# Kernel optimization log

Measured on AMD Instinct MI355X. Metric: run time of the kernel, lower is better.

The kernel has to match this reference:

```python
import jax, jax.numpy as jnp
import numpy as np

BN_EPS = 1e-5
TAU = 1.0  # gumbel temperature

def setup_inputs() -> dict:
    key = jax.random.key(0)
    ks = jax.random.split(key, 6)
    B, O, F, H, HID = 32, 4096, 256, 8, 128
    x = jax.random.normal(ks[0], (B, O, F), dtype=jnp.float32)
    gumbel_noise = jax.random.gumbel(ks[1], (B, O, H), dtype=jnp.float32)
    W_in = jax.random.normal(ks[2], (F, HID), dtype=jnp.float32) * (1.0 / np.sqrt(F))
    b_in = jnp.zeros((HID,), jnp.float32)
    W_blk = jax.random.normal(ks[3], (HID, HID), dtype=jnp.float32) * (1.0 / np.sqrt(HID))
    b_blk = jnp.zeros((HID,), jnp.float32)
    bn_gamma = jnp.ones((HID,), jnp.float32)
    bn_beta = jnp.zeros((HID,), jnp.float32)
    W_fc = jax.random.normal(ks[4], (HID, H), dtype=jnp.float32) * (1.0 / np.sqrt(HID))
    b_fc = jnp.zeros((H,), jnp.float32)
    return {"x": x, "gumbel_noise": gumbel_noise, "W_in": W_in, "b_in": b_in,
            "W_blk": W_blk, "b_blk": b_blk, "bn_gamma": bn_gamma, "bn_beta": bn_beta,
            "W_fc": W_fc, "b_fc": b_fc}

def reference(x, gumbel_noise, W_in, b_in, W_blk, b_blk, bn_gamma, bn_beta, W_fc, b_fc):
    B, O, F = x.shape
    xf = x.reshape(B * O, F)
    # DynamicNetwork head: input linear + relu, one residual block (Linear+BN+ReLU), fc
    h = jax.nn.relu(xf @ W_in + b_in)  # (B*O, HID)
    z = h @ W_blk + b_blk
    mu = z.mean(axis=0)
    var = z.var(axis=0)  # biased var, matches BatchNorm training normalization
    z = (z - mu) * jax.lax.rsqrt(var + BN_EPS) * bn_gamma + bn_beta
    h = jax.nn.relu(z) + h  # residual
    logits = (h @ W_fc + b_fc).reshape(B, O, -1)  # (B, O, H)
    # mask out zero-norm observations
    mask = (jnp.linalg.norm(x, axis=2) != 0)[..., None].astype(x.dtype)  # (B, O, 1)
    logits = logits * mask
    # gumbel softmax over observation dim (soft)
    w = jax.nn.softmax((logits + gumbel_noise) / TAU, axis=1)  # (B, O, H)
    # weighted sum pooling: algebraically the repeat-multiply-sum in the original
    pooled = jnp.einsum('boh,bof->bhf', w, x)  # (B, H, F)
    return pooled.reshape(B, -1)  # (B, H*F)
```

## Files before the change

kernel.cpp:

```cpp
#include <hip/hip_runtime.h>
#include <math.h>

#define MB_ 131072
#define F_  256
#define HID_ 128
#define H_  8
#define O_  4096
#define B_  32

typedef __attribute__((ext_vector_type(8))) short short8;
typedef __attribute__((ext_vector_type(4))) float f32x4;

static __device__ __forceinline__ unsigned short f2bf(float f) {
    unsigned int u = __float_as_uint(f);
    unsigned int r = (u + 0x7fffu + ((u >> 16) & 1u)) >> 16;
    return (unsigned short)r;
}
static __device__ __forceinline__ float bflo(unsigned int u) {
    return __uint_as_float(u << 16);
}
static __device__ __forceinline__ float bfhi(unsigned int u) {
    return __uint_as_float(u & 0xffff0000u);
}
static __device__ __forceinline__ unsigned int fkey(float f) {
    unsigned int u = __float_as_uint(f);
    return (u & 0x80000000u) ? ~u : (u | 0x80000000u);
}

__global__ __launch_bounds__(256) void k_prep(
    const float* __restrict__ W_in, const float* __restrict__ W_blk,
    unsigned short* __restrict__ WinT, unsigned short* __restrict__ WblkT,
    unsigned int* __restrict__ Mmax)
{
    const int idx = blockIdx.x * 256 + threadIdx.x;
    if (idx < 256) Mmax[idx] = 0u;
    if (idx < 32768) {
        const int n = idx >> 8, k = idx & 255;
        WinT[idx] = f2bf(W_in[(size_t)k * HID_ + n]);
    } else {
        const int i2 = idx - 32768;
        const int n = i2 >> 7, k = i2 & 127;
        WblkT[i2] = f2bf(W_blk[(size_t)k * HID_ + n]);
    }
}

__global__ __launch_bounds__(256) void k_fused(
    const float* __restrict__ x, const unsigned short* __restrict__ WinT,
    const float* __restrict__ b_in,
    const unsigned short* __restrict__ WblkT, const float* __restrict__ b_blk,
    unsigned short* __restrict__ h_out, unsigned short* __restrict__ z_out,
    float* __restrict__ mask_out,
    float* __restrict__ sumP, float* __restrict__ sumsqP)
{
    __shared__ unsigned short smem[128 * 136];
    __shared__ float msum_s[128];
    __shared__ float csum_s[128], csumsq_s[128];
    unsigned short* a_s = smem;
    unsigned short* b_s = smem + 5120;

    const int tid = threadIdx.x;
    const int R0 = blockIdx.x * 128;
    const int lp_r = tid >> 3;
    const int lp_c = tid & 7;
    const int wave = tid >> 6;
    const int wrow = wave >> 1, wcol = wave & 1;
    const int lane = tid & 63;
    const int lm = lane & 15, quad = lane >> 4;

    if (tid < 128) { msum_s[tid] = 0.f; csum_s[tid] = 0.f; csumsq_s[tid] = 0.f; }
    float ms[4] = {0.f, 0.f, 0.f, 0.f};

    f32x4 acc[4][4];
#pragma unroll
    for (int i = 0; i < 4; i++)
#pragma unroll
        for (int j = 0; j < 4; j++) acc[i][j] = (f32x4){0.f, 0.f, 0.f, 0.f};

    for (int kt = 0; kt < 8; kt++) {
#pragma unroll
        for (int p = 0; p < 4; p++) {
            const int r = lp_r + 32 * p;
            const float4 v = *(const float4*)(x + (size_t)(R0 + r) * F_ + kt * 32 + lp_c * 4);
            ms[p] += v.x * v.x + v.y * v.y + v.z * v.z + v.w * v.w;
            ushort4 o;
            o.x = f2bf(v.x); o.y = f2bf(v.y); o.z = f2bf(v.z); o.w = f2bf(v.w);
            *(ushort4*)(&a_s[r * 40 + lp_c * 4]) = o;
        }
#pragma unroll
        for (int p = 0; p < 4; p++) {
            const int n = lp_r + 32 * p;
            const ushort4 wv = *(const ushort4*)(WinT + (size_t)n * F_ + kt * 32 + lp_c * 4);
            *(ushort4*)(&b_s[n * 40 + lp_c * 4]) = wv;
        }
        __syncthreads();
        short8 af[4], bfr[4];
#pragma unroll
        for (int mi = 0; mi < 4; mi++)
            af[mi] = *(const short8*)(&a_s[(wrow * 64 + mi * 16 + lm) * 40 + quad * 8]);
#pragma unroll
        for (int ni = 0; ni < 4; ni++)
            bfr[ni] = *(const short8*)(&b_s[(wcol * 64 + ni * 16 + lm) * 40 + quad * 8]);
#pragma unroll
        for (int mi = 0; mi < 4; mi++)
#pragma unroll
            for (int ni = 0; ni < 4; ni++)
                acc[mi][ni] = __builtin_amdgcn_mfma_f32_16x16x32_bf16(af[mi], bfr[ni], acc[mi][ni], 0, 0, 0);
        __syncthreads();
    }

#pragma unroll
    for (int p = 0; p < 4; p++) atomicAdd(&msum_s[lp_r + 32 * p], ms[p]);

    {
        float bcol[4];
#pragma unroll
        for (int ni = 0; ni < 4; ni++) bcol[ni] = b_in[wcol * 64 + ni * 16 + lm];
#pragma unroll
        for (int mi = 0; mi < 4; mi++)
#pragma unroll
            for (int r = 0; r < 4; r++) {
                const int rl = wrow * 64 + mi * 16 + quad * 4 + r;
                const size_t grow = (size_t)(R0 + rl) * HID_;
#pragma unroll
                for (int ni = 0; ni < 4; ni++) {
                    const int col = wcol * 64 + ni * 16 + lm;
                    const float v = fmaxf(acc[mi][ni][r] + bcol[ni], 0.f);
                    const unsigned short us = f2bf(v);
                    h_out[grow + col] = us;
                    smem[rl * 136 + col] = us;
                }
            }
    }
#pragma unroll
    for (int i = 0; i < 4; i++)
#pragma unroll
        for (int j = 0; j < 4; j++) acc[i][j] = (f32x4){0.f, 0.f, 0.f, 0.f};
    __syncthreads();

    if (tid < 128) mask_out[R0 + tid] = (msum_s[tid] != 0.f) ? 1.f : 0.f;

#pragma unroll
    for (int kt = 0; kt < 4; kt++) {
        short8 af[4], bfr[4];
#pragma unroll
        for (int mi = 0; mi < 4; mi++)
            af[mi] = *(const short8*)(&smem[(wrow * 64 + mi * 16 + lm) * 136 + kt * 32 + quad * 8]);
#pragma unroll
        for (int ni = 0; ni < 4; ni++)
            bfr[ni] = *(const short8*)(WblkT + (size_t)(wcol * 64 + ni * 16 + lm) * HID_ + kt * 32 + quad * 8);
#pragma unroll
        for (int mi = 0; mi < 4; mi++)
#pragma unroll
            for (int ni = 0; ni < 4; ni++)
                acc[mi][ni] = __builtin_amdgcn_mfma_f32_16x16x32_bf16(af[mi], bfr[ni], acc[mi][ni], 0, 0, 0);
    }

    float bcol2[4];
#pragma unroll
    for (int ni = 0; ni < 4; ni++) bcol2[ni] = b_blk[wcol * 64 + ni * 16 + lm];
    float s_c[4] = {0.f, 0.f, 0.f, 0.f}, ss_c[4] = {0.f, 0.f, 0.f, 0.f};
#pragma unroll
    for (int mi = 0; mi < 4; mi++)
#pragma unroll
        for (int r = 0; r < 4; r++) {
            const size_t row = (size_t)R0 + wrow * 64 + mi * 16 + quad * 4 + r;
#pragma unroll
            for (int ni = 0; ni < 4; ni++) {
                const float zv = acc[mi][ni][r] + bcol2[ni];
                s_c[ni] += zv;
                ss_c[ni] += zv * zv;
                z_out[row * HID_ + wcol * 64 + ni * 16 + lm] = f2bf(zv);
            }
        }
#pragma unroll
    for (int ni = 0; ni < 4; ni++) {
        atomicAdd(&csum_s[wcol * 64 + ni * 16 + lm], s_c[ni]);
        atomicAdd(&csumsq_s[wcol * 64 + ni * 16 + lm], ss_c[ni]);
    }
    __syncthreads();
    if (tid < 128) {
        sumP[(size_t)blockIdx.x * 128 + tid] = csum_s[tid];
        sumsqP[(size_t)blockIdx.x * 128 + tid] = csumsq_s[tid];
    }
}

__global__ __launch_bounds__(256) void k_bnfin(
    const float* __restrict__ sumP, const float* __restrict__ sumsqP,
    const float* __restrict__ gamma, const float* __restrict__ beta,
    float* __restrict__ scale, float* __restrict__ shift)
{
    const int c = blockIdx.x;
    const int tid = threadIdx.x;
    float s = 0.f, ss = 0.f;
    for (int i = tid; i < 1024; i += 256) {
        s  += sumP[(size_t)i * 128 + c];
        ss += sumsqP[(size_t)i * 128 + c];
    }
#pragma unroll
    for (int off = 32; off; off >>= 1) {
        s  += __shfl_xor(s, off, 64);
        ss += __shfl_xor(ss, off, 64);
    }
    __shared__ float rs[4], rss[4];
    const int wid = tid >> 6, lane = tid & 63;
    if (lane == 0) { rs[wid] = s; rss[wid] = ss; }
    __syncthreads();
    if (tid == 0) {
        const float S  = rs[0] + rs[1] + rs[2] + rs[3];
        const float SS = rss[0] + rss[1] + rss[2] + rss[3];
        const float inv_m = 1.0f / (float)MB_;
        const float mu = S * inv_m;
        const float var = SS * inv_m - mu * mu;
        const float sc = gamma[c] * rsqrtf(var + 1e-5f);
        scale[c] = sc;
        shift[c] = beta[c] - mu * sc;
    }
}

__global__ __launch_bounds__(256) void k_logits(
    const unsigned short* __restrict__ h_in, const unsigned short* __restrict__ z_in,
    const float* __restrict__ scale, const float* __restrict__ shift,
    const float* __restrict__ W_fc, const float* __restrict__ b_fc,
    const float* __restrict__ mask, const float* __restrict__ gumbel,
    float* __restrict__ t_out, unsigned int* __restrict__ Mmax)
{
    __shared__ float wfc_s[1024];
    __shared__ float sc_s[128], sh_s[128];
    const int tid = threadIdx.x;
    for (int i = tid; i < 1024; i += 256) wfc_s[i] = W_fc[i];
    if (tid < 128) { sc_s[tid] = scale[tid]; sh_s[tid] = shift[tid]; }
    __syncthreads();

    const size_t row0 = (size_t)blockIdx.x * 512 + tid;
    const size_t row1 = row0 + 256;
    float a0[8], a1[8];
#pragma unroll
    for (int j = 0; j < 8; j++) { a0[j] = 0.f; a1[j] = 0.f; }

    const uint4* hp0 = (const uint4*)(h_in + row0 * HID_);
    const uint4* zq0 = (const uint4*)(z_in + row0 * HID_);
    const uint4* hp1 = (const uint4*)(h_in + row1 * HID_);
    const uint4* zq1 = (const uint4*)(z_in + row1 * HID_);

#pragma unroll 2
    for (int kc = 0; kc < 16; kc++) {
        const uint4 h0 = hp0[kc], z0 = zq0[kc];
        const uint4 h1 = hp1[kc], z1 = zq1[kc];
        const unsigned int hs0[4] = {h0.x, h0.y, h0.z, h0.w};
        const unsigned int zs0[4] = {z0.x, z0.y, z0.z, z0.w};
        const unsigned int hs1[4] = {h1.x, h1.y, h1.z, h1.w};
        const unsigned int zs1[4] = {z1.x, z1.y, z1.z, z1.w};
#pragma unroll
        for (int p = 0; p < 4; p++) {
            const int k = kc * 8 + p * 2;
            const float sck0 = sc_s[k], shk0 = sh_s[k];
            const float sck1 = sc_s[k + 1], shk1 = sh_s[k + 1];
            const float4 wA = *(const float4*)&wfc_s[k * 8];
            const float4 wB = *(const float4*)&wfc_s[k * 8 + 4];
            const float4 wC = *(const float4*)&wfc_s[k * 8 + 8];
            const float4 wD = *(const float4*)&wfc_s[k * 8 + 12];
            {
                const float hf0 = bflo(hs0[p]), hf1 = bfhi(hs0[p]);
                const float zf0 = bflo(zs0[p]), zf1 = bfhi(zs0[p]);
                const float hb0 = fmaxf(zf0 * sck0 + shk0, 0.f) + hf0;
                const float hb1 = fmaxf(zf1 * sck1 + shk1, 0.f) + hf1;
                a0[0] += hb0 * wA.x + hb1 * wC.x;  a0[1] += hb0 * wA.y + hb1 * wC.y;
                a0[2] += hb0 * wA.z + hb1 * wC.z;  a0[3] += hb0 * wA.w + hb1 * wC.w;
                a0[4] += hb0 * wB.x + hb1 * wD.x;  a0[5] += hb0 * wB.y + hb1 * wD.y;
                a0[6] += hb0 * wB.z + hb1 * wD.z;  a0[7] += hb0 * wB.w + hb1 * wD.w;
            }
            {
                const float hf0 = bflo(hs1[p]), hf1 = bfhi(hs1[p]);
                const float zf0 = bflo(zs1[p]), zf1 = bfhi(zs1[p]);
                const float hb0 = fmaxf(zf0 * sck0 + shk0, 0.f) + hf0;
                const float hb1 = fmaxf(zf1 * sck1 + shk1, 0.f) + hf1;
                a1[0] += hb0 * wA.x + hb1 * wC.x;  a1[1] += hb0 * wA.y + hb1 * wC.y;
                a1[2] += hb0 * wA.z + hb1 * wC.z;  a1[3] += hb0 * wA.w + hb1 * wC.w;
                a1[4] += hb0 * wB.x + hb1 * wD.x;  a1[5] += hb0 * wB.y + hb1 * wD.y;
                a1[6] += hb0 * wB.z + hb1 * wD.z;  a1[7] += hb0 * wB.w + hb1 * wD.w;
            }
        }
    }

    float bf[8];
#pragma unroll
    for (int j = 0; j < 8; j++) bf[j] = b_fc[j];
    const float mk0 = mask[row0], mk1 = mask[row1];
    float g0[8], g1[8];
    *(float4*)&g0[0] = *(const float4*)(gumbel + row0 * 8);
    *(float4*)&g0[4] = *(const float4*)(gumbel + row0 * 8 + 4);
    *(float4*)&g1[0] = *(const float4*)(gumbel + row1 * 8);
    *(float4*)&g1[4] = *(const float4*)(gumbel + row1 * 8 + 4);
    float t0[8], t1[8];
#pragma unroll
    for (int j = 0; j < 8; j++) {
        t0[j] = (a0[j] + bf[j]) * mk0 + g0[j];
        t1[j] = (a1[j] + bf[j]) * mk1 + g1[j];
    }
    *(float4*)(t_out + row0 * 8)     = *(float4*)&t0[0];
    *(float4*)(t_out + row0 * 8 + 4) = *(float4*)&t0[4];
    *(float4*)(t_out + row1 * 8)     = *(float4*)&t1[0];
    *(float4*)(t_out + row1 * 8 + 4) = *(float4*)&t1[4];

    float tm[8];
#pragma unroll
    for (int j = 0; j < 8; j++) tm[j] = fmaxf(t0[j], t1[j]);
#pragma unroll
    for (int off = 32; off; off >>= 1)
#pragma unroll
        for (int j = 0; j < 8; j++) tm[j] = fmaxf(tm[j], __shfl_xor(tm[j], off, 64));
    if ((tid & 63) == 0) {
        const int bb = blockIdx.x >> 3;
#pragma unroll
        for (int j = 0; j < 8; j++) atomicMax(&Mmax[bb * 8 + j], fkey(tm[j]));
    }
}

__global__ __launch_bounds__(256) void k_pool(
    const float* __restrict__ x, const float* __restrict__ t_in,
    const unsigned int* __restrict__ Mmax,
    float* __restrict__ pp, float* __restrict__ zp)
{
    __shared__ float ws_s[8][64];
    __shared__ float M_s[8];
    const int tid = threadIdx.x;
    const int oc = blockIdx.x;
    const int b  = blockIdx.y;
    if (tid < 8) {
        const unsigned int k = Mmax[b * 8 + tid];
        const unsigned int s = (k & 0x80000000u) ? (k & 0x7fffffffu) : ~k;
        M_s[tid] = __uint_as_float(s);
    }
    __syncthreads();
#pragma unroll
    for (int i = tid; i < 512; i += 256) {
        const int ol = i >> 3, hh = i & 7;
        const float tv = t_in[((size_t)b * O_ + oc * 64 + ol) * H_ + hh];
        ws_s[hh][ol] = __expf(tv - M_s[hh]);
    }
    __syncthreads();
    if (tid < 8) {
        float s = 0.f;
        for (int o = 0; o < 64; o++) s += ws_s[tid][o];
        zp[((size_t)oc * 32 + b) * 8 + tid] = s;
    }
    float acc[8];
#pragma unroll
    for (int hh = 0; hh < 8; hh++) acc[hh] = 0.f;
    const float* xp = x + ((size_t)b * O_ + oc * 64) * F_ + tid;
#pragma unroll 4
    for (int o = 0; o < 64; o++) {
        const float xv = xp[(size_t)o * F_];
#pragma unroll
        for (int hh = 0; hh < 8; hh++) acc[hh] += ws_s[hh][o] * xv;
    }
    float* outp = pp + ((size_t)oc * 32 + b) * 2048;
#pragma unroll
    for (int hh = 0; hh < 8; hh++) outp[hh * 256 + tid] = acc[hh];
}

__global__ __launch_bounds__(256) void k_reduce(
    const float* __restrict__ pp, const float* __restrict__ zp,
    float* __restrict__ out)
{
    const int blk = blockIdx.x;
    const int b = blk >> 3, hh = blk & 7;
    const int tid = threadIdx.x;
    __shared__ float invZ_s;
    if (tid < 64) {
        float z = zp[((size_t)tid * 32 + b) * 8 + hh];
#pragma unroll
        for (int off = 32; off; off >>= 1) z += __shfl_xor(z, off, 64);
        if (tid == 0) invZ_s = 1.f / z;
    }
    __syncthreads();
    float s = 0.f;
    const float* p0 = pp + (size_t)b * 2048 + hh * 256 + tid;
#pragma unroll 8
    for (int ocq = 0; ocq < 64; ocq++) s += p0[(size_t)ocq * 65536];
    out[(size_t)b * 2048 + hh * 256 + tid] = s * invZ_s;
}

extern "C" void kernel_launch(void* const* d_in, const int* in_sizes, int n_in,
                              void* d_out, int out_size, void* d_ws, size_t ws_size,
                              hipStream_t stream)
{
    const float* x      = (const float*)d_in[0];
    const float* gumbel = (const float*)d_in[1];
    const float* W_in   = (const float*)d_in[2];
    const float* b_in   = (const float*)d_in[3];
    const float* W_blk  = (const float*)d_in[4];
    const float* b_blk  = (const float*)d_in[5];
    const float* gamma  = (const float*)d_in[6];
    const float* beta   = (const float*)d_in[7];
    const float* W_fc   = (const float*)d_in[8];
    const float* b_fc   = (const float*)d_in[9];
    float* out = (float*)d_out;
    char* ws = (char*)d_ws;

    unsigned short* h_bf  = (unsigned short*)(ws + 0);
    float* pp     = (float*)(ws + 0);
    float* zp     = (float*)(ws + 16777216);
    unsigned short* z_bf  = (unsigned short*)(ws + 33554432);
    float* mask   = (float*)(ws + 67108864);
    float* sumP   = (float*)(ws + 67633152);
    float* sumsqP = (float*)(ws + 68157440);
    float* scale  = (float*)(ws + 68681728);
    float* shift  = (float*)(ws + 68682240);
    float* t_buf  = (float*)(ws + 68682752);
    unsigned int* Mmax = (unsigned int*)(ws + 72877056);
    unsigned short* WinT  = (unsigned short*)(ws + 72878080);
    unsigned short* WblkT = (unsigned short*)(ws + 72943616);

    k_prep<<<192, 256, 0, stream>>>(W_in, W_blk, WinT, WblkT, Mmax);
    k_fused<<<1024, 256, 0, stream>>>(x, WinT, b_in, WblkT, b_blk, h_bf, z_bf, mask, sumP, sumsqP);
    k_bnfin<<<128, 256, 0, stream>>>(sumP, sumsqP, gamma, beta, scale, shift);
    k_logits<<<256, 256, 0, stream>>>(h_bf, z_bf, scale, shift, W_fc, b_fc, mask, gumbel, t_buf, Mmax);
    k_pool<<<dim3(64, 32), 256, 0, stream>>>(x, t_buf, Mmax, pp, zp);
    k_reduce<<<256, 256, 0, stream>>>(pp, zp, out);
}
```

Before: 304.9 us.

## Double-width k_fused with 512 threads, register prefetch of next K tile

The fused first-stage GEMM kernel now runs 512 threads (8 waves in a 2x4 grid, each wave owning a 64x32 tile), uses a 64-wide K step instead of 32, and loads the next x/W_in slice into registers while MFMAs run on the current LDS tile. It also preloads the W_blk fragments into registers before the second GEMM so those global loads overlap the h epilogue. The intent is to hide global load latency and halve the number of barriers per tile, at the cost of more register pressure and a larger LDS footprint, which could limit occupancy.

```diff
diff --git a/kernel.cpp b/kernel.cpp
--- a/kernel.cpp
+++ b/kernel.cpp
@@ -44,7 +44,7 @@
     }
 }
 
-__global__ __launch_bounds__(256) void k_fused(
+__global__ __launch_bounds__(512, 4) void k_fused(
     const float* __restrict__ x, const unsigned short* __restrict__ WinT,
     const float* __restrict__ b_in,
     const unsigned short* __restrict__ WblkT, const float* __restrict__ b_blk,
@@ -52,69 +52,95 @@
     float* __restrict__ mask_out,
     float* __restrict__ sumP, float* __restrict__ sumsqP)
 {
-    __shared__ unsigned short smem[128 * 136];
+    __shared__ unsigned short smem[128 * 144];
     __shared__ float msum_s[128];
     __shared__ float csum_s[128], csumsq_s[128];
     unsigned short* a_s = smem;
-    unsigned short* b_s = smem + 5120;
+    unsigned short* b_s = smem + 128 * 72;
 
     const int tid = threadIdx.x;
     const int R0 = blockIdx.x * 128;
-    const int lp_r = tid >> 3;
-    const int lp_c = tid & 7;
+    const int sr = tid >> 2;
+    const int sc = tid & 3;
     const int wave = tid >> 6;
-    const int wrow = wave >> 1, wcol = wave & 1;
+    const int wrow = wave >> 2;
+    const int wcol = wave & 3;
     const int lane = tid & 63;
     const int lm = lane & 15, quad = lane >> 4;
 
     if (tid < 128) { msum_s[tid] = 0.f; csum_s[tid] = 0.f; csumsq_s[tid] = 0.f; }
-    float ms[4] = {0.f, 0.f, 0.f, 0.f};
-
-    f32x4 acc[4][4];
+    float ms = 0.f;
+
+    f32x4 acc[4][2];
 #pragma unroll
     for (int i = 0; i < 4; i++)
 #pragma unroll
-        for (int j = 0; j < 4; j++) acc[i][j] = (f32x4){0.f, 0.f, 0.f, 0.f};
-
-    for (int kt = 0; kt < 8; kt++) {
-#pragma unroll
-        for (int p = 0; p < 4; p++) {
-            const int r = lp_r + 32 * p;
-            const float4 v = *(const float4*)(x + (size_t)(R0 + r) * F_ + kt * 32 + lp_c * 4);
-            ms[p] += v.x * v.x + v.y * v.y + v.z * v.z + v.w * v.w;
+        for (int j = 0; j < 2; j++) acc[i][j] = (f32x4){0.f, 0.f, 0.f, 0.f};
+
+    float4 ax[4];
+    short8 bxr[2];
+#pragma unroll
+    for (int q = 0; q < 4; q++)
+        ax[q] = *(const float4*)(x + (size_t)(R0 + sr) * F_ + (q * 4 + sc) * 4);
+#pragma unroll
+    for (int q = 0; q < 2; q++)
+        bxr[q] = *(const short8*)(WinT + (size_t)sr * F_ + (sc + 4 * q) * 8);
+
+#pragma unroll
+    for (int kt = 0; kt < 4; kt++) {
+#pragma unroll
+        for (int q = 0; q < 4; q++) {
+            const float4 v = ax[q];
+            ms += v.x * v.x + v.y * v.y + v.z * v.z + v.w * v.w;
             ushort4 o;
             o.x = f2bf(v.x); o.y = f2bf(v.y); o.z = f2bf(v.z); o.w = f2bf(v.w);
-            *(ushort4*)(&a_s[r * 40 + lp_c * 4]) = o;
+            *(ushort4*)(&a_s[sr * 72 + (q * 4 + sc) * 4]) = o;
         }
 #pragma unroll
-        for (int p = 0; p < 4; p++) {
-            const int n = lp_r + 32 * p;
-            const ushort4 wv = *(const ushort4*)(WinT + (size_t)n * F_ + kt * 32 + lp_c * 4);
-            *(ushort4*)(&b_s[n * 40 + lp_c * 4]) = wv;
+        for (int q = 0; q < 2; q++)
+            *(short8*)(&b_s[sr * 72 + (sc + 4 * q) * 8]) = bxr[q];
+        __syncthreads();
+
+        if (kt < 3) {
+#pragma unroll
+            for (int q = 0; q < 4; q++)
+                ax[q] = *(const float4*)(x + (size_t)(R0 + sr) * F_ + (kt + 1) * 64 + (q * 4 + sc) * 4);
+#pragma unroll
+            for (int q = 0; q < 2; q++)
+                bxr[q] = *(const short8*)(WinT + (size_t)sr * F_ + (kt + 1) * 64 + (sc + 4 * q) * 8);
+        }
+
+#pragma unroll
+        for (int ks = 0; ks < 2; ks++) {
+            short8 af[4], bfr[2];
+#pragma unroll
+            for (int mi = 0; mi < 4; mi++)
+                af[mi] = *(const short8*)(&a_s[(wrow * 64 + mi * 16 + lm) * 72 + ks * 32 + quad * 8]);
+#pragma unroll
+            for (int ni = 0; ni < 2; ni++)
+                bfr[ni] = *(const short8*)(&b_s[(wcol * 32 + ni * 16 + lm) * 72 + ks * 32 + quad * 8]);
+#pragma unroll
+            for (int mi = 0; mi < 4; mi++)
+#pragma unroll
+                for (int ni = 0; ni < 2; ni++)
+                    acc[mi][ni] = __builtin_amdgcn_mfma_f32_16x16x32_bf16(af[mi], bfr[ni], acc[mi][ni], 0, 0, 0);
         }
         __syncthreads();
-        short8 af[4], bfr[4];
-#pragma unroll
-        for (int mi = 0; mi < 4; mi++)
-            af[mi] = *(const short8*)(&a_s[(wrow * 64 + mi * 16 + lm) * 40 + quad * 8]);
-#pragma unroll
-        for (int ni = 0; ni < 4; ni++)
-            bfr[ni] = *(const short8*)(&b_s[(wcol * 64 + ni * 16 + lm) * 40 + quad * 8]);
-#pragma unroll
-        for (int mi = 0; mi < 4; mi++)
-#pragma unroll
-            for (int ni = 0; ni < 4; ni++)
-                acc[mi][ni] = __builtin_amdgcn_mfma_f32_16x16x32_bf16(af[mi], bfr[ni], acc[mi][ni], 0, 0, 0);
-        __syncthreads();
-    }
-
-#pragma unroll
-    for (int p = 0; p < 4; p++) atomicAdd(&msum_s[lp_r + 32 * p], ms[p]);
+    }
+
+    atomicAdd(&msum_s[sr], ms);
+
+    short8 wb[4][2];
+#pragma unroll
+    for (int kt2 = 0; kt2 < 4; kt2++)
+#pragma unroll
+        for (int ni = 0; ni < 2; ni++)
+            wb[kt2][ni] = *(const short8*)(WblkT + (size_t)(wcol * 32 + ni * 16 + lm) * HID_ + kt2 * 32 + quad * 8);
 
     {
-        float bcol[4];
-#pragma unroll
-        for (int ni = 0; ni < 4; ni++) bcol[ni] = b_in[wcol * 64 + ni * 16 + lm];
+        float bcol[2];
+#pragma unroll
+        for (int ni = 0; ni < 2; ni++) bcol[ni] = b_in[wcol * 32 + ni * 16 + lm];
 #pragma unroll
         for (int mi = 0; mi < 4; mi++)
 #pragma unroll
@@ -122,8 +148,8 @@
                 const int rl = wrow * 64 + mi * 16 + quad * 4 + r;
                 const size_t grow = (size_t)(R0 + rl) * HID_;
 #pragma unroll
-                for (int ni = 0; ni < 4; ni++) {
-                    const int col = wcol * 64 + ni * 16 + lm;
+                for (int ni = 0; ni < 2; ni++) {
+                    const int col = wcol * 32 + ni * 16 + lm;
                     const float v = fmaxf(acc[mi][ni][r] + bcol[ni], 0.f);
                     const unsigned short us = f2bf(v);
                     h_out[grow + col] = us;
@@ -134,48 +160,45 @@
 #pragma unroll
     for (int i = 0; i < 4; i++)
 #pragma unroll
-        for (int j = 0; j < 4; j++) acc[i][j] = (f32x4){0.f, 0.f, 0.f, 0.f};
+        for (int j = 0; j < 2; j++) acc[i][j] = (f32x4){0.f, 0.f, 0.f, 0.f};
     __syncthreads();
 
     if (tid < 128) mask_out[R0 + tid] = (msum_s[tid] != 0.f) ? 1.f : 0.f;
 
 #pragma unroll
-    for (int kt = 0; kt < 4; kt++) {
-        short8 af[4], bfr[4];
+    for (int kt2 = 0; kt2 < 4; kt2++) {
+        short8 haf[4];
 #pragma unroll
         for (int mi = 0; mi < 4; mi++)
-            af[mi] = *(const short8*)(&smem[(wrow * 64 + mi * 16 + lm) * 136 + kt * 32 + quad * 8]);
-#pragma unroll
-        for (int ni = 0; ni < 4; ni++)
-            bfr[ni] = *(const short8*)(WblkT + (size_t)(wcol * 64 + ni * 16 + lm) * HID_ + kt * 32 + quad * 8);
+            haf[mi] = *(const short8*)(&smem[(wrow * 64 + mi * 16 + lm) * 136 + kt2 * 32 + quad * 8]);
 #pragma unroll
         for (int mi = 0; mi < 4; mi++)
 #pragma unroll
-            for (int ni = 0; ni < 4; ni++)
-                acc[mi][ni] = __builtin_amdgcn_mfma_f32_16x16x32_bf16(af[mi], bfr[ni], acc[mi][ni], 0, 0, 0);
-    }
-
-    float bcol2[4];
-#pragma unroll
-    for (int ni = 0; ni < 4; ni++) bcol2[ni] = b_blk[wcol * 64 + ni * 16 + lm];
-    float s_c[4] = {0.f, 0.f, 0.f, 0.f}, ss_c[4] = {0.f, 0.f, 0.f, 0.f};
+            for (int ni = 0; ni < 2; ni++)
+                acc[mi][ni] = __builtin_amdgcn_mfma_f32_16x16x32_bf16(haf[mi], wb[kt2][ni], acc[mi][ni], 0, 0, 0);
+    }
+
+    float bcol2[2];
+#pragma unroll
+    for (int ni = 0; ni < 2; ni++) bcol2[ni] = b_blk[wcol * 32 + ni * 16 + lm];
+    float s_c[2] = {0.f, 0.f}, ss_c[2] = {0.f, 0.f};
 #pragma unroll
     for (int mi = 0; mi < 4; mi++)
 #pragma unroll
         for (int r = 0; r < 4; r++) {
             const size_t row = (size_t)R0 + wrow * 64 + mi * 16 + quad * 4 + r;
 #pragma unroll
-            for (int ni = 0; ni < 4; ni++) {
+            for (int ni = 0; ni < 2; ni++) {
                 const float zv = acc[mi][ni][r] + bcol2[ni];
                 s_c[ni] += zv;
                 ss_c[ni] += zv * zv;
-                z_out[row * HID_ + wcol * 64 + ni * 16 + lm] = f2bf(zv);
+                z_out[row * HID_ + wcol * 32 + ni * 16 + lm] = f2bf(zv);
             }
         }
 #pragma unroll
-    for (int ni = 0; ni < 4; ni++) {
-        atomicAdd(&csum_s[wcol * 64 + ni * 16 + lm], s_c[ni]);
-        atomicAdd(&csumsq_s[wcol * 64 + ni * 16 + lm], ss_c[ni]);
+    for (int ni = 0; ni < 2; ni++) {
+        atomicAdd(&csum_s[wcol * 32 + ni * 16 + lm], s_c[ni]);
+        atomicAdd(&csumsq_s[wcol * 32 + ni * 16 + lm], ss_c[ni]);
     }
     __syncthreads();
     if (tid < 128) {
@@ -413,7 +436,7 @@
     unsigned short* WblkT = (unsigned short*)(ws + 72943616);
 
     k_prep<<<192, 256, 0, stream>>>(W_in, W_blk, WinT, WblkT, Mmax);
-    k_fused<<<1024, 256, 0, stream>>>(x, WinT, b_in, WblkT, b_blk, h_bf, z_bf, mask, sumP, sumsqP);
+    k_fused<<<1024, 512, 0, stream>>>(x, WinT, b_in, WblkT, b_blk, h_bf, z_bf, mask, sumP, sumsqP);
     k_bnfin<<<128, 256, 0, stream>>>(sumP, sumsqP, gamma, beta, scale, shift);
     k_logits<<<256, 256, 0, stream>>>(h_bf, z_bf, scale, shift, W_fc, b_fc, mask, gumbel, t_buf, Mmax);
     k_pool<<<dim3(64, 32), 256, 0, stream>>>(x, t_buf, Mmax, pp, zp);
```

Result: no change. 303.6 us (-0.4%).
